# Kernel optimization log

Measured on AMD Instinct MI355X. Metric: run time of the kernel, lower is better.

Reference implementation:

```python
import jax, jax.numpy as jnp
import numpy as np

GROUP_SIZE = 64
SHARED_EXPERT_WEIGHT = 1.0
# FP4 E2M1 codebook: sign bit + {0,.5,1,1.5,2,3,4,6}
FP4_TABLE = jnp.array([0.0, 0.5, 1.0, 1.5, 2.0, 3.0, 4.0, 6.0,
                       -0.0, -0.5, -1.0, -1.5, -2.0, -3.0, -4.0, -6.0], dtype=jnp.float32)


def dequant_fp4(packed, scales, group_size=GROUP_SIZE):
    """packed: [..., K//8, N] int32 (8 nibbles along K per word),
    scales: [..., K//group_size, N] -> dequantized [..., K, N] fp32."""
    shifts = (jnp.arange(8, dtype=jnp.int32) * 4)[:, None]          # [8,1]
    nib = jnp.right_shift(packed[..., :, None, :], shifts) & 0xF     # [..., K//8, 8, N]
    w = FP4_TABLE[nib]
    K = packed.shape[-2] * 8
    w = w.reshape(packed.shape[:-2] + (K, packed.shape[-1]))         # [..., K, N]
    s = jnp.repeat(scales, group_size, axis=-2)                      # [..., K, N]
    return w * s


def setup_inputs() -> dict:
    key = jax.random.key(0)
    ks = jax.random.split(key, 12)
    T, K, I, E, TOPK = 2048, 2048, 1024, 8, 2
    GS = GROUP_SIZE
    MAXI = 2**31 - 1
    u = lambda k, shp: jax.random.uniform(k, shp, jnp.float32, 0.005, 0.02)
    probs = jax.random.uniform(ks[10], (T, TOPK), jnp.float32)
    probs = probs / probs.sum(-1, keepdims=True)
    return {
        "hidden_states": jax.random.normal(ks[0], (T, K), jnp.float32),
        "gate_up_weight_packed": jax.random.randint(ks[1], (E, K // 8, 2 * I), 0, MAXI, jnp.int32),
        "gate_up_scales": u(ks[2], (E, K // GS, 2 * I)),
        "down_weight_packed": jax.random.randint(ks[3], (E, I // 8, K), 0, MAXI, jnp.int32),
        "down_scales": u(ks[4], (E, I // GS, K)),
        "shared_gate_up_packed": jax.random.randint(ks[5], (K // 8, 2 * I), 0, MAXI, jnp.int32),
        "shared_gate_up_scales": u(ks[6], (K // GS, 2 * I)),
        "shared_down_packed": jax.random.randint(ks[7], (I // 8, K), 0, MAXI, jnp.int32),
        "shared_down_scales": u(ks[8], (I // GS, K)),
        "expert_ids": jax.random.randint(ks[9], (T, TOPK), 0, E, jnp.int32),
        "expert_probs": probs,
    }


def reference(hidden_states, gate_up_weight_packed, gate_up_scales,
              down_weight_packed, down_scales,
              shared_gate_up_packed, shared_gate_up_scales,
              shared_down_packed, shared_down_scales,
              expert_ids, expert_probs):
    x = hidden_states                                                # [T, K]
    E = gate_up_weight_packed.shape[0]
    # --- routed experts: dequant + grouped GEMM over all tokens per expert ---
    Wgu = dequant_fp4(gate_up_weight_packed, gate_up_scales)         # [E, K, 2I]
    Wd = dequant_fp4(down_weight_packed, down_scales)                # [E, I, K]
    h = jnp.einsum('tk,ekn->etn', x, Wgu)                            # [E, T, 2I]
    gate, up = jnp.split(h, 2, axis=-1)
    act = jax.nn.silu(gate) * up                                     # [E, T, I]
    y = jnp.einsum('eti,eik->etk', act, Wd)                          # [E, T, K]
    # combine[t,e] = sum over top-k slots routed to e of prob
    one_hot = jax.nn.one_hot(expert_ids, E, dtype=x.dtype)           # [T, topk, E]
    combine = jnp.einsum('tk,tke->te', expert_probs, one_hot)        # [T, E]
    out = jnp.einsum('te,etk->tk', combine, y)                       # [T, K]
    # --- shared expert (always applied, weighted) ---
    Wgu_s = dequant_fp4(shared_gate_up_packed, shared_gate_up_scales)  # [K, 2I]
    Wd_s = dequant_fp4(shared_down_packed, shared_down_scales)         # [I, K]
    hs = x @ Wgu_s
    gs, us = jnp.split(hs, 2, axis=-1)
    shared_out = (jax.nn.silu(gs) * us) @ Wd_s
    return out + SHARED_EXPERT_WEIGHT * shared_out
```

## Files before the change

### kernel.cpp

```cpp
#include <hip/hip_runtime.h>
#include <hip/hip_fp16.h>

#define T_TOK 2048
#define K_DIM 2048
#define I_DIM 1024
#define NE    8
#define TOPK  2
#define GS    64

#define NSLOT  (T_TOK * TOPK)
#define TOTROW (NSLOT + T_TOK)
#define MAXITEM 32

typedef __attribute__((ext_vector_type(8))) _Float16 half8;
typedef __attribute__((ext_vector_type(4))) float f32x4;

#define WS_XB   ((size_t)65536)
#define WS_ACT  (WS_XB  + (size_t)2048 * 2048 * 2)
#define WS_Y    (WS_ACT + (size_t)TOTROW * 1024 * 2)


__device__ __forceinline__ float h2f(ushort h) {
    __half v = *reinterpret_cast<__half*>(&h);
    return __half2float(v);
}

__device__ __forceinline__ void dq_word(unsigned w, __half2 S, unsigned o[4]) {
    unsigned lo  = w & 0x0F0F0F0Fu;
    unsigned hi  = (w >> 4) & 0x0F0F0F0Fu;
    unsigned mlo = lo & 0x07070707u, mhi = hi & 0x07070707u;
    unsigned Hlo = __builtin_amdgcn_perm(0x46444240u, 0x3E3C3800u, mlo)
                 | ((lo & 0x08080808u) << 4);
    unsigned Hhi = __builtin_amdgcn_perm(0x46444240u, 0x3E3C3800u, mhi)
                 | ((hi & 0x08080808u) << 4);
    unsigned e01 = __builtin_amdgcn_perm(Hlo, 0u, 0x05000400u);
    unsigned e23 = __builtin_amdgcn_perm(Hlo, 0u, 0x07000600u);
    unsigned o01 = __builtin_amdgcn_perm(Hhi, 0u, 0x05000400u);
    unsigned o23 = __builtin_amdgcn_perm(Hhi, 0u, 0x07000600u);
    __half2 v0 = __hmul2(*reinterpret_cast<__half2*>(&e01), S);
    __half2 v1 = __hmul2(*reinterpret_cast<__half2*>(&e23), S);
    __half2 v2 = __hmul2(*reinterpret_cast<__half2*>(&o01), S);
    __half2 v3 = __hmul2(*reinterpret_cast<__half2*>(&o23), S);
    o[0] = *reinterpret_cast<unsigned*>(&v0);
    o[1] = *reinterpret_cast<unsigned*>(&v1);
    o[2] = *reinterpret_cast<unsigned*>(&v2);
    o[3] = *reinterpret_cast<unsigned*>(&v3);
}

__device__ __forceinline__ void gld16(const void* g, void* l) {
    __builtin_amdgcn_global_load_lds(
        (const __attribute__((address_space(1))) unsigned*)g,
        (__attribute__((address_space(3))) unsigned*)l, 16, 0, 0);
}

#define PREP_BLK 2048
#define FRONT_GRID (PREP_BLK + 1)

__global__ __launch_bounds__(256) void k_front(
        const float* __restrict__ x, ushort* __restrict__ xb,
        const int* __restrict__ eids,
        int* __restrict__ gcnt, int* __restrict__ gbase,
        int* __restrict__ tileCnt, int* __restrict__ tileE, int* __restrict__ tileM,
        int* __restrict__ tok, int* __restrict__ inv) {
    int id = blockIdx.x;
    int tid = threadIdx.x;

    if (id < PREP_BLK) {
        int idx = id * 256 + tid;
        const float4* p = (const float4*)(x + (size_t)idx * 8);
        float4 f0 = p[0], f1 = p[1];
        __half2 h0 = __floats2half2_rn(f0.x, f0.z);
        __half2 h1 = __floats2half2_rn(f1.x, f1.z);
        __half2 h2 = __floats2half2_rn(f0.y, f0.w);
        __half2 h3 = __floats2half2_rn(f1.y, f1.w);
        unsigned u0 = *reinterpret_cast<unsigned*>(&h0);
        unsigned u1 = *reinterpret_cast<unsigned*>(&h1);
        unsigned u2 = *reinterpret_cast<unsigned*>(&h2);
        unsigned u3 = *reinterpret_cast<unsigned*>(&h3);
        *(int4*)(xb + (size_t)idx * 8) = make_int4(u0, u1, u2, u3);
    } else {
        __shared__ int lcnt[NE], lbase[NE], lcur[NE];
        if (tid < NE) lcnt[tid] = 0;
        __syncthreads();
        for (int i = tid; i < NSLOT; i += 256)
            atomicAdd(&lcnt[eids[i]], 1);
        __syncthreads();
        if (tid == 0) {
            int acc = 0;
            for (int e = 0; e < NE; e++) { lbase[e] = acc; acc += lcnt[e]; }
        }
        __syncthreads();
        if (tid < NE) lcur[tid] = lbase[tid];
        __syncthreads();
        for (int i = tid; i < NSLOT; i += 256) {
            int e = eids[i];
            int pos = atomicAdd(&lcur[e], 1);
            tok[pos] = i >> 1;
            inv[i] = pos;
        }
        for (int t = tid; t < T_TOK; t += 256)
            tok[NSLOT + t] = t;
        if (tid < NE) { gcnt[tid] = lcnt[tid]; gbase[tid] = lbase[tid]; }
        if (tid == 0) {
            gcnt[NE] = T_TOK; gbase[NE] = NSLOT;
            int nt = 0;
            for (int e = 0; e < NE + 1; e++) {
                int c = (e < NE) ? lcnt[e] : T_TOK;
                for (int m = 0; m < c; m += 256) { tileE[nt] = e; tileM[nt] = m; nt++; }
            }
            *tileCnt = nt;
            for (int i = nt; i < 64; i++) { tileE[i] = 0; tileM[i] = 0; }
        }
    }
}

__global__ __launch_bounds__(512) void k_gemm_gateup(
        const ushort* __restrict__ xb,
        const int* __restrict__ gup, const float* __restrict__ gus,
        const int* __restrict__ sup, const float* __restrict__ sus,
        const int* __restrict__ gcnt, const int* __restrict__ gbase,
        const int* __restrict__ tileCnt, const int* __restrict__ tileE,
        const int* __restrict__ tileM,
        const int* __restrict__ tokid, ushort* __restrict__ act) {
    int item = blockIdx.y;
    if (item >= *tileCnt) return;
    int tid = threadIdx.x;
    int e = tileE[item], m0 = tileM[item];
    int cnt = gcnt[e], base = gbase[e];
    int n0 = blockIdx.x * 64;
    const int* wp; const float* sc;
    if (e < NE) { wp = gup + (size_t)e * 256 * 2048; sc = gus + (size_t)e * 32 * 2048; }
    else        { wp = sup; sc = sus; }

    __shared__ __align__(16) ushort xs[256 * 64];
    __shared__ __align__(16) ushort bs[128 * 64];

    int lane = tid & 63, wv = tid >> 6;
    int lid = lane & 15, quad = lane >> 4;
    int wr = wv >> 1, wc = wv & 1;
    int l8 = lane >> 3, l7 = lane & 7;
    int chunk = (l7 ^ l8) * 8;

    const ushort* aSrc[4];
    #pragma unroll
    for (int it = 0; it < 4; it++) {
        int rA = wv * 32 + it * 8 + l8;
        int t = (m0 + rA < cnt) ? tokid[base + m0 + rA] : 0;
        aSrc[it] = xb + (size_t)t * K_DIM + chunk;
    }

    int nloc = tid & 127;
    int kw0 = (tid >> 7) * 2;
    int bj = nloc & 63, bh = nloc >> 6;
    int ncol = (bj < 32) ? (n0 + bh * 32 + bj) : (I_DIM + n0 + bh * 32 + (bj - 32));
    int bd0 = nloc * 64 + ((kw0    ) ^ (nloc & 7)) * 8;
    int bd1 = nloc * 64 + ((kw0 + 1) ^ (nloc & 7)) * 8;

    const int NT = K_DIM / 64;
    const int* wq = wp + (size_t)kw0 * 2048 + ncol;
    const float* sq = sc + ncol;
    unsigned w0 = (unsigned)wq[0];
    unsigned w1 = (unsigned)wq[2048];
    float s = *sq;
    wq += 16384; sq += 2048;

    f32x4 acc[4][4] = {};

    for (int t = 0; t < NT; ++t) {
        #pragma unroll
        for (int it = 0; it < 4; it++) {
            gld16(aSrc[it], &xs[(wv * 4 + it) * 512]);
            aSrc[it] += 64;
        }
        {
            __half2 S = __half2half2(__float2half(s));
            unsigned o[4];
            dq_word(w0, S, o); *(int4*)&bs[bd0] = make_int4(o[0], o[1], o[2], o[3]);
            dq_word(w1, S, o); *(int4*)&bs[bd1] = make_int4(o[0], o[1], o[2], o[3]);
        }
        if (t + 1 < NT) {
            w0 = (unsigned)wq[0];
            w1 = (unsigned)wq[2048];
            s = *sq;
            wq += 16384; sq += 2048;
        }
        __syncthreads();
        __builtin_amdgcn_s_setprio(1);
        #pragma unroll
        for (int ks = 0; ks < 2; ks++) {
            int slot = ((ks * 4 + quad) ^ l7) * 8;
            half8 a[4], b[4];
            #pragma unroll
            for (int mt = 0; mt < 4; mt++)
                a[mt] = *(const half8*)&xs[(wr * 64 + mt * 16 + lid) * 64 + slot];
            #pragma unroll
            for (int nt = 0; nt < 4; nt++)
                b[nt] = *(const half8*)&bs[(wc * 64 + nt * 16 + lid) * 64 + slot];
            #pragma unroll
            for (int mt = 0; mt < 4; mt++)
                #pragma unroll
                for (int nt = 0; nt < 4; nt++)
                    acc[mt][nt] = __builtin_amdgcn_mfma_f32_16x16x32_f16(
                        a[mt], b[nt], acc[mt][nt], 0, 0, 0);
        }
        __builtin_amdgcn_s_setprio(0);
        __syncthreads();
    }

    int c7 = lid & 7;
    int delta = ((c7 >> 1) + ((c7 & 1) << 2)) - c7;
    #pragma unroll
    for (int mt = 0; mt < 4; mt++) {
        #pragma unroll
        for (int i = 0; i < 4; i++) {
            int row = wr * 64 + mt * 16 + quad * 4 + i;
            if (m0 + row < cnt) {
                size_t p = (size_t)(base + m0 + row);
                #pragma unroll
                for (int nt = 0; nt < 2; nt++) {
                    float g = acc[mt][nt][i], u = acc[mt][nt + 2][i];
                    float vv = g / (1.f + __expf(-g)) * u;
                    int ncol2 = n0 + wc * 32 + nt * 16 + lid;
                    __half hb = __float2half(vv);
                    act[p * I_DIM + ncol2 + delta] = *reinterpret_cast<ushort*>(&hb);
                }
            }
        }
    }
}

__global__ __launch_bounds__(512) void k_gemm_down(
        const ushort* __restrict__ actb,
        const int* __restrict__ dwp, const float* __restrict__ dsc,
        const int* __restrict__ sdp, const float* __restrict__ sds,
        const int* __restrict__ gcnt, const int* __restrict__ gbase,
        const int* __restrict__ tileCnt, const int* __restrict__ tileE,
        const int* __restrict__ tileM,
        ushort* __restrict__ y) {
    int item = blockIdx.y;
    if (item >= *tileCnt) return;
    int tid = threadIdx.x;
    int e = tileE[item], m0 = tileM[item];
    int cnt = gcnt[e], base = gbase[e];
    int n0 = blockIdx.x * 128;
    const int* wp; const float* sc;
    if (e < NE) { wp = dwp + (size_t)e * 128 * 2048; sc = dsc + (size_t)e * 16 * 2048; }
    else        { wp = sdp; sc = sds; }

    __shared__ __align__(16) ushort xs[256 * 64];
    __shared__ __align__(16) ushort bs[128 * 64];

    int lane = tid & 63, wv = tid >> 6;
    int lid = lane & 15, quad = lane >> 4;
    int wr = wv >> 1, wc = wv & 1;
    int l8 = lane >> 3, l7 = lane & 7;
    int chunk = (l7 ^ l8) * 8;

    const ushort* aSrc[4];
    #pragma unroll
    for (int it = 0; it < 4; it++) {
        int rA = wv * 32 + it * 8 + l8;
        int rr = m0 + rA; if (rr >= cnt) rr = cnt - 1;
        aSrc[it] = actb + (size_t)(base + rr) * I_DIM + chunk;
    }

    int nloc = tid & 127;
    int kw0 = (tid >> 7) * 2;
    int ncol = n0 + nloc;
    int bd0 = nloc * 64 + ((kw0    ) ^ (nloc & 7)) * 8;
    int bd1 = nloc * 64 + ((kw0 + 1) ^ (nloc & 7)) * 8;

    const int NT = I_DIM / 64;
    const int* wq = wp + (size_t)kw0 * 2048 + ncol;
    const float* sq = sc + ncol;
    unsigned w0 = (unsigned)wq[0];
    unsigned w1 = (unsigned)wq[2048];
    float s = *sq;
    wq += 16384; sq += 2048;

    f32x4 acc[4][4] = {};

    for (int t = 0; t < NT; ++t) {
        #pragma unroll
        for (int it = 0; it < 4; it++) {
            gld16(aSrc[it], &xs[(wv * 4 + it) * 512]);
            aSrc[it] += 64;
        }
        {
            __half2 S = __half2half2(__float2half(s));
            unsigned o[4];
            dq_word(w0, S, o); *(int4*)&bs[bd0] = make_int4(o[0], o[1], o[2], o[3]);
            dq_word(w1, S, o); *(int4*)&bs[bd1] = make_int4(o[0], o[1], o[2], o[3]);
        }
        if (t + 1 < NT) {
            w0 = (unsigned)wq[0];
            w1 = (unsigned)wq[2048];
            s = *sq;
            wq += 16384; sq += 2048;
        }
        __syncthreads();
        __builtin_amdgcn_s_setprio(1);
        #pragma unroll
        for (int ks = 0; ks < 2; ks++) {
            int slot = ((ks * 4 + quad) ^ l7) * 8;
            half8 a[4], b[4];
            #pragma unroll
            for (int mt = 0; mt < 4; mt++)
                a[mt] = *(const half8*)&xs[(wr * 64 + mt * 16 + lid) * 64 + slot];
            #pragma unroll
            for (int nt = 0; nt < 4; nt++)
                b[nt] = *(const half8*)&bs[(wc * 64 + nt * 16 + lid) * 64 + slot];
            #pragma unroll
            for (int mt = 0; mt < 4; mt++)
                #pragma unroll
                for (int nt = 0; nt < 4; nt++)
                    acc[mt][nt] = __builtin_amdgcn_mfma_f32_16x16x32_f16(
                        a[mt], b[nt], acc[mt][nt], 0, 0, 0);
        }
        __builtin_amdgcn_s_setprio(0);
        __syncthreads();
    }

    #pragma unroll
    for (int mt = 0; mt < 4; mt++) {
        #pragma unroll
        for (int i = 0; i < 4; i++) {
            int row = wr * 64 + mt * 16 + quad * 4 + i;
            if (m0 + row < cnt) {
                ushort* yrow = y + (size_t)(base + m0 + row) * 2048 + n0 + wc * 64 + lid;
                #pragma unroll
                for (int nt = 0; nt < 4; nt++) {
                    __half hb = __float2half(acc[mt][nt][i]);
                    yrow[nt * 16] = *reinterpret_cast<ushort*>(&hb);
                }
            }
        }
    }
}

__global__ __launch_bounds__(256) void k_combine(
        const ushort* __restrict__ y, const int* __restrict__ inv,
        const float* __restrict__ prb, float* __restrict__ out) {
    int idx = blockIdx.x * 256 + threadIdx.x;
    int t = idx >> 8;
    int c = (idx & 255) * 8;
    int p0 = inv[2 * t], p1 = inv[2 * t + 1];
    float w0 = prb[2 * t], w1 = prb[2 * t + 1];
    int4 a = *(const int4*)(y + (size_t)p0 * 2048 + c);
    int4 b = *(const int4*)(y + (size_t)p1 * 2048 + c);
    int4 s = *(const int4*)(y + (size_t)(NSLOT + t) * 2048 + c);
    const ushort* au = (const ushort*)&a;
    const ushort* bu = (const ushort*)&b;
    const ushort* su = (const ushort*)&s;
    float o[8];
    #pragma unroll
    for (int j = 0; j < 8; j++)
        o[j] = w0 * h2f(au[j]) + w1 * h2f(bu[j]) + h2f(su[j]);
    *(float4*)(out + (size_t)t * 2048 + c)     = *(float4*)&o[0];
    *(float4*)(out + (size_t)t * 2048 + c + 4) = *(float4*)&o[4];
}

extern "C" void kernel_launch(void* const* d_in, const int* in_sizes, int n_in,
                              void* d_out, int out_size, void* d_ws, size_t ws_size,
                              hipStream_t stream) {
    const float* x    = (const float*)d_in[0];
    const int*   gup  = (const int*)d_in[1];
    const float* gus  = (const float*)d_in[2];
    const int*   dwp  = (const int*)d_in[3];
    const float* dsc  = (const float*)d_in[4];
    const int*   sup  = (const int*)d_in[5];
    const float* sus  = (const float*)d_in[6];
    const int*   sdp  = (const int*)d_in[7];
    const float* sds  = (const float*)d_in[8];
    const int*   eids = (const int*)d_in[9];
    const float* prb  = (const float*)d_in[10];
    float* out = (float*)d_out;

    char*   ws      = (char*)d_ws;
    int*    gcnt    = (int*)(ws + 0);
    int*    gbase   = (int*)(ws + 64);
    int*    tileCnt = (int*)(ws + 128);
    int*    tileE   = (int*)(ws + 192);
    int*    tileM   = (int*)(ws + 448);
    int*    tok     = (int*)(ws + 1024);
    int*    inv     = (int*)(ws + 25600);
    ushort* xb      = (ushort*)(ws + WS_XB);
    ushort* act     = (ushort*)(ws + WS_ACT);
    ushort* y       = (ushort*)(ws + WS_Y);

    k_front<<<FRONT_GRID, 256, 0, stream>>>(
        x, xb, eids, gcnt, gbase, tileCnt, tileE, tileM, tok, inv);
    k_gemm_gateup<<<dim3(I_DIM / 64, MAXITEM), 512, 0, stream>>>(
        xb, gup, gus, sup, sus, gcnt, gbase, tileCnt, tileE, tileM, tok, act);
    k_gemm_down<<<dim3(K_DIM / 128, MAXITEM), 512, 0, stream>>>(
        act, dwp, dsc, sdp, sds, gcnt, gbase, tileCnt, tileE, tileM, y);
    k_combine<<<(T_TOK * K_DIM / 8) / 256, 256, 0, stream>>>(y, inv, prb, out);
}
```

Baseline: 228.9 us.

## Shrink GEMM tiles to 256x64 with 4 waves and move weight prefetch after barrier

Both grouped GEMM kernels change from 512-thread blocks with 256x128 tiles to 256-thread blocks with 256x64 tiles. Each wave now owns 64 rows across the full N width, and the grid doubles along N. The next weight word prefetch is moved after the first barrier into temporaries, with a sched_barrier, so its load latency overlaps the MFMA loop. Smaller tiles and launch_bounds(256,3) aim for more resident blocks and better occupancy, at the cost of reloading A tiles twice as often and dequantizing the same weights less efficiently per FLOP.

Result: slower. 241.2 us (+5.3%).

```diff
diff --git a/kernel.cpp b/kernel.cpp
--- a/kernel.cpp
+++ b/kernel.cpp
@@ -114,7 +114,7 @@
     }
 }
 
-__global__ __launch_bounds__(512) void k_gemm_gateup(
+__global__ __launch_bounds__(256, 3) void k_gemm_gateup(
         const ushort* __restrict__ xb,
         const int* __restrict__ gup, const float* __restrict__ gus,
         const int* __restrict__ sup, const float* __restrict__ sus,
@@ -127,34 +127,32 @@
     int tid = threadIdx.x;
     int e = tileE[item], m0 = tileM[item];
     int cnt = gcnt[e], base = gbase[e];
-    int n0 = blockIdx.x * 64;
+    int n0 = blockIdx.x * 32;
     const int* wp; const float* sc;
     if (e < NE) { wp = gup + (size_t)e * 256 * 2048; sc = gus + (size_t)e * 32 * 2048; }
     else        { wp = sup; sc = sus; }
 
     __shared__ __align__(16) ushort xs[256 * 64];
-    __shared__ __align__(16) ushort bs[128 * 64];
+    __shared__ __align__(16) ushort bs[64 * 64];
 
     int lane = tid & 63, wv = tid >> 6;
     int lid = lane & 15, quad = lane >> 4;
-    int wr = wv >> 1, wc = wv & 1;
     int l8 = lane >> 3, l7 = lane & 7;
     int chunk = (l7 ^ l8) * 8;
 
-    const ushort* aSrc[4];
+    const ushort* aSrc[8];
     #pragma unroll
-    for (int it = 0; it < 4; it++) {
-        int rA = wv * 32 + it * 8 + l8;
+    for (int it = 0; it < 8; it++) {
+        int rA = wv * 64 + it * 8 + l8;
         int t = (m0 + rA < cnt) ? tokid[base + m0 + rA] : 0;
         aSrc[it] = xb + (size_t)t * K_DIM + chunk;
     }
 
-    int nloc = tid & 127;
-    int kw0 = (tid >> 7) * 2;
-    int bj = nloc & 63, bh = nloc >> 6;
-    int ncol = (bj < 32) ? (n0 + bh * 32 + bj) : (I_DIM + n0 + bh * 32 + (bj - 32));
-    int bd0 = nloc * 64 + ((kw0    ) ^ (nloc & 7)) * 8;
-    int bd1 = nloc * 64 + ((kw0 + 1) ^ (nloc & 7)) * 8;
+    int col = tid & 63;
+    int kw0 = (tid >> 6) * 2;
+    int ncol = (col < 32) ? (n0 + col) : (I_DIM + n0 + (col - 32));
+    int bd0 = col * 64 + ((kw0    ) ^ (col & 7)) * 8;
+    int bd1 = col * 64 + ((kw0 + 1) ^ (col & 7)) * 8;
 
     const int NT = K_DIM / 64;
     const int* wq = wp + (size_t)kw0 * 2048 + ncol;
@@ -168,8 +166,8 @@
 
     for (int t = 0; t < NT; ++t) {
         #pragma unroll
-        for (int it = 0; it < 4; it++) {
-            gld16(aSrc[it], &xs[(wv * 4 + it) * 512]);
+        for (int it = 0; it < 8; it++) {
+            gld16(aSrc[it], &xs[(wv * 8 + it) * 512]);
             aSrc[it] += 64;
         }
         {
@@ -178,13 +176,15 @@
             dq_word(w0, S, o); *(int4*)&bs[bd0] = make_int4(o[0], o[1], o[2], o[3]);
             dq_word(w1, S, o); *(int4*)&bs[bd1] = make_int4(o[0], o[1], o[2], o[3]);
         }
+        __syncthreads();
+        unsigned nw0 = w0, nw1 = w1; float ns = s;
         if (t + 1 < NT) {
-            w0 = (unsigned)wq[0];
-            w1 = (unsigned)wq[2048];
-            s = *sq;
+            nw0 = (unsigned)wq[0];
+            nw1 = (unsigned)wq[2048];
+            ns = *sq;
             wq += 16384; sq += 2048;
         }
-        __syncthreads();
+        __builtin_amdgcn_sched_barrier(0);
         __builtin_amdgcn_s_setprio(1);
         #pragma unroll
         for (int ks = 0; ks < 2; ks++) {
@@ -192,10 +192,10 @@
             half8 a[4], b[4];
             #pragma unroll
             for (int mt = 0; mt < 4; mt++)
-                a[mt] = *(const half8*)&xs[(wr * 64 + mt * 16 + lid) * 64 + slot];
+                a[mt] = *(const half8*)&xs[(wv * 64 + mt * 16 + lid) * 64 + slot];
             #pragma unroll
             for (int nt = 0; nt < 4; nt++)
-                b[nt] = *(const half8*)&bs[(wc * 64 + nt * 16 + lid) * 64 + slot];
+                b[nt] = *(const half8*)&bs[(nt * 16 + lid) * 64 + slot];
             #pragma unroll
             for (int mt = 0; mt < 4; mt++)
                 #pragma unroll
@@ -205,6 +205,7 @@
         }
         __builtin_amdgcn_s_setprio(0);
         __syncthreads();
+        w0 = nw0; w1 = nw1; s = ns;
     }
 
     int c7 = lid & 7;
@@ -213,14 +214,14 @@
     for (int mt = 0; mt < 4; mt++) {
         #pragma unroll
         for (int i = 0; i < 4; i++) {
-            int row = wr * 64 + mt * 16 + quad * 4 + i;
+            int row = wv * 64 + mt * 16 + quad * 4 + i;
             if (m0 + row < cnt) {
                 size_t p = (size_t)(base + m0 + row);
                 #pragma unroll
                 for (int nt = 0; nt < 2; nt++) {
                     float g = acc[mt][nt][i], u = acc[mt][nt + 2][i];
                     float vv = g / (1.f + __expf(-g)) * u;
-                    int ncol2 = n0 + wc * 32 + nt * 16 + lid;
+                    int ncol2 = n0 + nt * 16 + lid;
                     __half hb = __float2half(vv);
                     act[p * I_DIM + ncol2 + delta] = *reinterpret_cast<ushort*>(&hb);
                 }
@@ -229,7 +230,7 @@
     }
 }
 
-__global__ __launch_bounds__(512) void k_gemm_down(
+__global__ __launch_bounds__(256, 3) void k_gemm_down(
         const ushort* __restrict__ actb,
         const int* __restrict__ dwp, const float* __restrict__ dsc,
         const int* __restrict__ sdp, const float* __restrict__ sds,
@@ -242,33 +243,32 @@
     int tid = threadIdx.x;
     int e = tileE[item], m0 = tileM[item];
     int cnt = gcnt[e], base = gbase[e];
-    int n0 = blockIdx.x * 128;
+    int n0 = blockIdx.x * 64;
     const int* wp; const float* sc;
     if (e < NE) { wp = dwp + (size_t)e * 128 * 2048; sc = dsc + (size_t)e * 16 * 2048; }
     else        { wp = sdp; sc = sds; }
 
     __shared__ __align__(16) ushort xs[256 * 64];
-    __shared__ __align__(16) ushort bs[128 * 64];
+    __shared__ __align__(16) ushort bs[64 * 64];
 
     int lane = tid & 63, wv = tid >> 6;
     int lid = lane & 15, quad = lane >> 4;
-    int wr = wv >> 1, wc = wv & 1;
     int l8 = lane >> 3, l7 = lane & 7;
     int chunk = (l7 ^ l8) * 8;
 
-    const ushort* aSrc[4];
+    const ushort* aSrc[8];
     #pragma unroll
-    for (int it = 0; it < 4; it++) {
-        int rA = wv * 32 + it * 8 + l8;
+    for (int it = 0; it < 8; it++) {
+        int rA = wv * 64 + it * 8 + l8;
         int rr = m0 + rA; if (rr >= cnt) rr = cnt - 1;
         aSrc[it] = actb + (size_t)(base + rr) * I_DIM + chunk;
     }
 
-    int nloc = tid & 127;
-    int kw0 = (tid >> 7) * 2;
-    int ncol = n0 + nloc;
-    int bd0 = nloc * 64 + ((kw0    ) ^ (nloc & 7)) * 8;
-    int bd1 = nloc * 64 + ((kw0 + 1) ^ (nloc & 7)) * 8;
+    int col = tid & 63;
+    int kw0 = (tid >> 6) * 2;
+    int ncol = n0 + col;
+    int bd0 = col * 64 + ((kw0    ) ^ (col & 7)) * 8;
+    int bd1 = col * 64 + ((kw0 + 1) ^ (col & 7)) * 8;
 
     const int NT = I_DIM / 64;
     const int* wq = wp + (size_t)kw0 * 2048 + ncol;
@@ -282,8 +282,8 @@
 
     for (int t = 0; t < NT; ++t) {
         #pragma unroll
-        for (int it = 0; it < 4; it++) {
-            gld16(aSrc[it], &xs[(wv * 4 + it) * 512]);
+        for (int it = 0; it < 8; it++) {
+            gld16(aSrc[it], &xs[(wv * 8 + it) * 512]);
             aSrc[it] += 64;
         }
         {
@@ -292,13 +292,15 @@
             dq_word(w0, S, o); *(int4*)&bs[bd0] = make_int4(o[0], o[1], o[2], o[3]);
             dq_word(w1, S, o); *(int4*)&bs[bd1] = make_int4(o[0], o[1], o[2], o[3]);
         }
+        __syncthreads();
+        unsigned nw0 = w0, nw1 = w1; float ns = s;
         if (t + 1 < NT) {
-            w0 = (unsigned)wq[0];
-            w1 = (unsigned)wq[2048];
-            s = *sq;
+            nw0 = (unsigned)wq[0];
+            nw1 = (unsigned)wq[2048];
+            ns = *sq;
             wq += 16384; sq += 2048;
         }
-        __syncthreads();
+        __builtin_amdgcn_sched_barrier(0);
         __builtin_amdgcn_s_setprio(1);
         #pragma unroll
         for (int ks = 0; ks < 2; ks++) {
@@ -306,10 +308,10 @@
             half8 a[4], b[4];
             #pragma unroll
             for (int mt = 0; mt < 4; mt++)
-                a[mt] = *(const half8*)&xs[(wr * 64 + mt * 16 + lid) * 64 + slot];
+                a[mt] = *(const half8*)&xs[(wv * 64 + mt * 16 + lid) * 64 + slot];
             #pragma unroll
             for (int nt = 0; nt < 4; nt++)
-                b[nt] = *(const half8*)&bs[(wc * 64 + nt * 16 + lid) * 64 + slot];
+                b[nt] = *(const half8*)&bs[(nt * 16 + lid) * 64 + slot];
             #pragma unroll
             for (int mt = 0; mt < 4; mt++)
                 #pragma unroll
@@ -319,15 +321,16 @@
         }
         __builtin_amdgcn_s_setprio(0);
         __syncthreads();
+        w0 = nw0; w1 = nw1; s = ns;
     }
 
     #pragma unroll
     for (int mt = 0; mt < 4; mt++) {
         #pragma unroll
         for (int i = 0; i < 4; i++) {
-            int row = wr * 64 + mt * 16 + quad * 4 + i;
+            int row = wv * 64 + mt * 16 + quad * 4 + i;
             if (m0 + row < cnt) {
-                ushort* yrow = y + (size_t)(base + m0 + row) * 2048 + n0 + wc * 64 + lid;
+                ushort* yrow = y + (size_t)(base + m0 + row) * 2048 + n0 + lid;
                 #pragma unroll
                 for (int nt = 0; nt < 4; nt++) {
                     __half hb = __float2half(acc[mt][nt][i]);
@@ -390,9 +393,9 @@
 
     k_front<<<FRONT_GRID, 256, 0, stream>>>(
         x, xb, eids, gcnt, gbase, tileCnt, tileE, tileM, tok, inv);
-    k_gemm_gateup<<<dim3(I_DIM / 64, MAXITEM), 512, 0, stream>>>(
+    k_gemm_gateup<<<dim3(I_DIM / 32, MAXITEM), 256, 0, stream>>>(
         xb, gup, gus, sup, sus, gcnt, gbase, tileCnt, tileE, tileM, tok, act);
-    k_gemm_down<<<dim3(K_DIM / 128, MAXITEM), 512, 0, stream>>>(
+    k_gemm_down<<<dim3(K_DIM / 64, MAXITEM), 256, 0, stream>>>(
         act, dwp, dsc, sdp, sds, gcnt, gbase, tileCnt, tileE, tileM, y);
     k_combine<<<(T_TOK * K_DIM / 8) / 256, 256, 0, stream>>>(y, inv, prb, out);
 }
```

## Fuse combine into down GEMM epilogue via weighted atomic adds to output

Applied to the files above, without the earlier changes.

Removes the separate combine kernel and the fp16 intermediate y buffer. The front kernel now zeroes the output and stores a per-row routing weight (1.0 for shared-expert rows). The down GEMM epilogue scatters weighted fp32 atomicAdds directly into the output rows by token id. This saves one kernel launch and the write plus reread of roughly 25 MB of intermediates. In exchange it adds three-way atomic contention per output element, uncoalesced scalar atomics, and a summation order that is no longer deterministic.

Measured after the change: 255.5 us. 1.12x slower.

```diff
diff --git a/kernel.cpp b/kernel.cpp
--- a/kernel.cpp
+++ b/kernel.cpp
@@ -17,13 +17,7 @@
 
 #define WS_XB   ((size_t)65536)
 #define WS_ACT  (WS_XB  + (size_t)2048 * 2048 * 2)
-#define WS_Y    (WS_ACT + (size_t)TOTROW * 1024 * 2)
-
-
-__device__ __forceinline__ float h2f(ushort h) {
-    __half v = *reinterpret_cast<__half*>(&h);
-    return __half2float(v);
-}
+
 
 __device__ __forceinline__ void dq_word(unsigned w, __half2 S, unsigned o[4]) {
     unsigned lo  = w & 0x0F0F0F0Fu;
@@ -58,10 +52,11 @@
 
 __global__ __launch_bounds__(256) void k_front(
         const float* __restrict__ x, ushort* __restrict__ xb,
-        const int* __restrict__ eids,
+        const int* __restrict__ eids, const float* __restrict__ prb,
+        float* __restrict__ out,
         int* __restrict__ gcnt, int* __restrict__ gbase,
         int* __restrict__ tileCnt, int* __restrict__ tileE, int* __restrict__ tileM,
-        int* __restrict__ tok, int* __restrict__ inv) {
+        int* __restrict__ tok, float* __restrict__ wgt) {
     int id = blockIdx.x;
     int tid = threadIdx.x;
 
@@ -78,6 +73,9 @@
         unsigned u2 = *reinterpret_cast<unsigned*>(&h2);
         unsigned u3 = *reinterpret_cast<unsigned*>(&h3);
         *(int4*)(xb + (size_t)idx * 8) = make_int4(u0, u1, u2, u3);
+        float4 z = make_float4(0.f, 0.f, 0.f, 0.f);
+        *(float4*)(out + (size_t)idx * 8)     = z;
+        *(float4*)(out + (size_t)idx * 8 + 4) = z;
     } else {
         __shared__ int lcnt[NE], lbase[NE], lcur[NE];
         if (tid < NE) lcnt[tid] = 0;
@@ -96,10 +94,12 @@
             int e = eids[i];
             int pos = atomicAdd(&lcur[e], 1);
             tok[pos] = i >> 1;
-            inv[i] = pos;
-        }
-        for (int t = tid; t < T_TOK; t += 256)
+            wgt[pos] = prb[i];
+        }
+        for (int t = tid; t < T_TOK; t += 256) {
             tok[NSLOT + t] = t;
+            wgt[NSLOT + t] = 1.0f;
+        }
         if (tid < NE) { gcnt[tid] = lcnt[tid]; gbase[tid] = lbase[tid]; }
         if (tid == 0) {
             gcnt[NE] = T_TOK; gbase[NE] = NSLOT;
@@ -236,7 +236,8 @@
         const int* __restrict__ gcnt, const int* __restrict__ gbase,
         const int* __restrict__ tileCnt, const int* __restrict__ tileE,
         const int* __restrict__ tileM,
-        ushort* __restrict__ y) {
+        const int* __restrict__ tokid, const float* __restrict__ wgt,
+        float* __restrict__ out) {
     int item = blockIdx.y;
     if (item >= *tileCnt) return;
     int tid = threadIdx.x;
@@ -327,37 +328,16 @@
         for (int i = 0; i < 4; i++) {
             int row = wr * 64 + mt * 16 + quad * 4 + i;
             if (m0 + row < cnt) {
-                ushort* yrow = y + (size_t)(base + m0 + row) * 2048 + n0 + wc * 64 + lid;
+                int p = base + m0 + row;
+                int tkn = tokid[p];
+                float w = wgt[p];
+                float* orow = out + (size_t)tkn * 2048 + n0 + wc * 64 + lid;
                 #pragma unroll
-                for (int nt = 0; nt < 4; nt++) {
-                    __half hb = __float2half(acc[mt][nt][i]);
-                    yrow[nt * 16] = *reinterpret_cast<ushort*>(&hb);
-                }
+                for (int nt = 0; nt < 4; nt++)
+                    atomicAdd(&orow[nt * 16], w * acc[mt][nt][i]);
             }
         }
     }
-}
-
-__global__ __launch_bounds__(256) void k_combine(
-        const ushort* __restrict__ y, const int* __restrict__ inv,
-        const float* __restrict__ prb, float* __restrict__ out) {
-    int idx = blockIdx.x * 256 + threadIdx.x;
-    int t = idx >> 8;
-    int c = (idx & 255) * 8;
-    int p0 = inv[2 * t], p1 = inv[2 * t + 1];
-    float w0 = prb[2 * t], w1 = prb[2 * t + 1];
-    int4 a = *(const int4*)(y + (size_t)p0 * 2048 + c);
-    int4 b = *(const int4*)(y + (size_t)p1 * 2048 + c);
-    int4 s = *(const int4*)(y + (size_t)(NSLOT + t) * 2048 + c);
-    const ushort* au = (const ushort*)&a;
-    const ushort* bu = (const ushort*)&b;
-    const ushort* su = (const ushort*)&s;
-    float o[8];
-    #pragma unroll
-    for (int j = 0; j < 8; j++)
-        o[j] = w0 * h2f(au[j]) + w1 * h2f(bu[j]) + h2f(su[j]);
-    *(float4*)(out + (size_t)t * 2048 + c)     = *(float4*)&o[0];
-    *(float4*)(out + (size_t)t * 2048 + c + 4) = *(float4*)&o[4];
 }
 
 extern "C" void kernel_launch(void* const* d_in, const int* in_sizes, int n_in,
@@ -383,16 +363,14 @@
     int*    tileE   = (int*)(ws + 192);
     int*    tileM   = (int*)(ws + 448);
     int*    tok     = (int*)(ws + 1024);
-    int*    inv     = (int*)(ws + 25600);
+    float*  wgt     = (float*)(ws + 25600);
     ushort* xb      = (ushort*)(ws + WS_XB);
     ushort* act     = (ushort*)(ws + WS_ACT);
-    ushort* y       = (ushort*)(ws + WS_Y);
 
     k_front<<<FRONT_GRID, 256, 0, stream>>>(
-        x, xb, eids, gcnt, gbase, tileCnt, tileE, tileM, tok, inv);
+        x, xb, eids, prb, out, gcnt, gbase, tileCnt, tileE, tileM, tok, wgt);
     k_gemm_gateup<<<dim3(I_DIM / 64, MAXITEM), 512, 0, stream>>>(
         xb, gup, gus, sup, sus, gcnt, gbase, tileCnt, tileE, tileM, tok, act);
     k_gemm_down<<<dim3(K_DIM / 128, MAXITEM), 512, 0, stream>>>(
-        act, dwp, dsc, sdp, sds, gcnt, gbase, tileCnt, tileE, tileM, y);
-    k_combine<<<(T_TOK * K_DIM / 8) / 256, 256, 0, stream>>>(y, inv, prb, out);
-}
+        act, dwp, dsc, sdp, sds, gcnt, gbase, tileCnt, tileE, tileM, tok, wgt, out);
+}
```

## Fuse all MoE stages into one cooperative persistent kernel with grid syncs

Applied to the files above, without the earlier changes.

Replaces the four separate launches (convert/route, gate-up GEMM, down GEMM, combine) with a single cooperative kernel of 512 blocks that separates the stages with grid.sync. Each block handles one tile item per GEMM phase (bid>>4 indexes the item), and the conversion and combine phases use grid-stride loops. The aim is to remove launch gaps and tail effects between kernels. In exchange, the grid is capped at 512 blocks, which limits parallelism per phase, and it adds the cost of grid-wide barriers. If the cooperative launch fails, it falls back to the old four-kernel path.

New measurement: 429.2 us. 87.5% more time.

```diff
diff --git a/kernel.cpp b/kernel.cpp
--- a/kernel.cpp
+++ b/kernel.cpp
@@ -1,5 +1,8 @@
 #include <hip/hip_runtime.h>
 #include <hip/hip_fp16.h>
+#include <hip/hip_cooperative_groups.h>
+
+namespace cg = cooperative_groups;
 
 #define T_TOK 2048
 #define K_DIM 2048
@@ -53,6 +56,303 @@
         (__attribute__((address_space(3))) unsigned*)l, 16, 0, 0);
 }
 
+#define FGRID 512
+
+__global__ __launch_bounds__(512, 4) void k_fused(
+        const float* __restrict__ x,
+        const int* __restrict__ gup, const float* __restrict__ gus,
+        const int* __restrict__ dwp, const float* __restrict__ dsc,
+        const int* __restrict__ sup, const float* __restrict__ sus,
+        const int* __restrict__ sdp, const float* __restrict__ sds,
+        const int* __restrict__ eids, const float* __restrict__ prb,
+        float* __restrict__ out,
+        ushort* __restrict__ xb, ushort* __restrict__ act, ushort* __restrict__ y,
+        int* __restrict__ gcnt, int* __restrict__ gbase,
+        int* __restrict__ tileCnt, int* __restrict__ tileE, int* __restrict__ tileM,
+        int* __restrict__ tok, int* __restrict__ inv) {
+    cg::grid_group grid = cg::this_grid();
+    const int bid = blockIdx.x;
+    const int tid = threadIdx.x;
+
+    __shared__ __align__(16) ushort xs[256 * 64];
+    __shared__ __align__(16) ushort bs[128 * 64];
+
+    for (int idx = bid * 512 + tid; idx < T_TOK * K_DIM / 8; idx += FGRID * 512) {
+        const float4* p = (const float4*)(x + (size_t)idx * 8);
+        float4 f0 = p[0], f1 = p[1];
+        __half2 h0 = __floats2half2_rn(f0.x, f0.z);
+        __half2 h1 = __floats2half2_rn(f1.x, f1.z);
+        __half2 h2 = __floats2half2_rn(f0.y, f0.w);
+        __half2 h3 = __floats2half2_rn(f1.y, f1.w);
+        *(int4*)(xb + (size_t)idx * 8) = make_int4(
+            *reinterpret_cast<unsigned*>(&h0), *reinterpret_cast<unsigned*>(&h1),
+            *reinterpret_cast<unsigned*>(&h2), *reinterpret_cast<unsigned*>(&h3));
+    }
+    if (bid == 0) {
+        int* lcnt  = (int*)xs;
+        int* lbase = lcnt + 8;
+        int* lcur  = lbase + 8;
+        if (tid < NE) lcnt[tid] = 0;
+        __syncthreads();
+        for (int i = tid; i < NSLOT; i += 512)
+            atomicAdd(&lcnt[eids[i]], 1);
+        __syncthreads();
+        if (tid == 0) {
+            int acc = 0;
+            for (int e = 0; e < NE; e++) { lbase[e] = acc; acc += lcnt[e]; }
+        }
+        __syncthreads();
+        if (tid < NE) lcur[tid] = lbase[tid];
+        __syncthreads();
+        for (int i = tid; i < NSLOT; i += 512) {
+            int e = eids[i];
+            int pos = atomicAdd(&lcur[e], 1);
+            tok[pos] = i >> 1;
+            inv[i] = pos;
+        }
+        for (int t = tid; t < T_TOK; t += 512)
+            tok[NSLOT + t] = t;
+        if (tid < NE) { gcnt[tid] = lcnt[tid]; gbase[tid] = lbase[tid]; }
+        if (tid == 0) {
+            gcnt[NE] = T_TOK; gbase[NE] = NSLOT;
+            int nt = 0;
+            for (int e = 0; e < NE + 1; e++) {
+                int c = (e < NE) ? lcnt[e] : T_TOK;
+                for (int m = 0; m < c; m += 256) { tileE[nt] = e; tileM[nt] = m; nt++; }
+            }
+            *tileCnt = nt;
+            for (int i = nt; i < 64; i++) { tileE[i] = 0; tileM[i] = 0; }
+        }
+    }
+    grid.sync();
+
+    {
+        int item = bid >> 4;
+        if (item < *tileCnt) {
+            int e = tileE[item], m0 = tileM[item];
+            int cnt = gcnt[e], base = gbase[e];
+            int n0 = (bid & 15) * 64;
+            const int* wp; const float* sc;
+            if (e < NE) { wp = gup + (size_t)e * 256 * 2048; sc = gus + (size_t)e * 32 * 2048; }
+            else        { wp = sup; sc = sus; }
+
+            int lane = tid & 63, wv = tid >> 6;
+            int lid = lane & 15, quad = lane >> 4;
+            int wr = wv >> 1, wc = wv & 1;
+            int l8 = lane >> 3, l7 = lane & 7;
+            int chunk = (l7 ^ l8) * 8;
+
+            const ushort* aSrc[4];
+            #pragma unroll
+            for (int it = 0; it < 4; it++) {
+                int rA = wv * 32 + it * 8 + l8;
+                int t = (m0 + rA < cnt) ? tok[base + m0 + rA] : 0;
+                aSrc[it] = xb + (size_t)t * K_DIM + chunk;
+            }
+
+            int nloc = tid & 127;
+            int kw0 = (tid >> 7) * 2;
+            int bj = nloc & 63, bh = nloc >> 6;
+            int ncol = (bj < 32) ? (n0 + bh * 32 + bj) : (I_DIM + n0 + bh * 32 + (bj - 32));
+            int bd0 = nloc * 64 + ((kw0    ) ^ (nloc & 7)) * 8;
+            int bd1 = nloc * 64 + ((kw0 + 1) ^ (nloc & 7)) * 8;
+
+            const int NT = K_DIM / 64;
+            const int* wq = wp + (size_t)kw0 * 2048 + ncol;
+            const float* sq = sc + ncol;
+            unsigned w0 = (unsigned)wq[0];
+            unsigned w1 = (unsigned)wq[2048];
+            float s = *sq;
+            wq += 16384; sq += 2048;
+
+            f32x4 acc[4][4] = {};
+
+            for (int t = 0; t < NT; ++t) {
+                #pragma unroll
+                for (int it = 0; it < 4; it++) {
+                    gld16(aSrc[it], &xs[(wv * 4 + it) * 512]);
+                    aSrc[it] += 64;
+                }
+                {
+                    __half2 S = __half2half2(__float2half(s));
+                    unsigned o[4];
+                    dq_word(w0, S, o); *(int4*)&bs[bd0] = make_int4(o[0], o[1], o[2], o[3]);
+                    dq_word(w1, S, o); *(int4*)&bs[bd1] = make_int4(o[0], o[1], o[2], o[3]);
+                }
+                if (t + 1 < NT) {
+                    w0 = (unsigned)wq[0];
+                    w1 = (unsigned)wq[2048];
+                    s = *sq;
+                    wq += 16384; sq += 2048;
+                }
+                __syncthreads();
+                __builtin_amdgcn_s_setprio(1);
+                #pragma unroll
+                for (int ks = 0; ks < 2; ks++) {
+                    int slot = ((ks * 4 + quad) ^ l7) * 8;
+                    half8 a[4], b[4];
+                    #pragma unroll
+                    for (int mt = 0; mt < 4; mt++)
+                        a[mt] = *(const half8*)&xs[(wr * 64 + mt * 16 + lid) * 64 + slot];
+                    #pragma unroll
+                    for (int nt = 0; nt < 4; nt++)
+                        b[nt] = *(const half8*)&bs[(wc * 64 + nt * 16 + lid) * 64 + slot];
+                    #pragma unroll
+                    for (int mt = 0; mt < 4; mt++)
+                        #pragma unroll
+                        for (int nt = 0; nt < 4; nt++)
+                            acc[mt][nt] = __builtin_amdgcn_mfma_f32_16x16x32_f16(
+                                a[mt], b[nt], acc[mt][nt], 0, 0, 0);
+                }
+                __builtin_amdgcn_s_setprio(0);
+                __syncthreads();
+            }
+
+            int c7 = lid & 7;
+            int delta = ((c7 >> 1) + ((c7 & 1) << 2)) - c7;
+            #pragma unroll
+            for (int mt = 0; mt < 4; mt++) {
+                #pragma unroll
+                for (int i = 0; i < 4; i++) {
+                    int row = wr * 64 + mt * 16 + quad * 4 + i;
+                    if (m0 + row < cnt) {
+                        size_t p = (size_t)(base + m0 + row);
+                        #pragma unroll
+                        for (int nt = 0; nt < 2; nt++) {
+                            float g = acc[mt][nt][i], u = acc[mt][nt + 2][i];
+                            float vv = g / (1.f + __expf(-g)) * u;
+                            int ncol2 = n0 + wc * 32 + nt * 16 + lid;
+                            __half hb = __float2half(vv);
+                            act[p * I_DIM + ncol2 + delta] = *reinterpret_cast<ushort*>(&hb);
+                        }
+                    }
+                }
+            }
+        }
+    }
+    grid.sync();
+
+    {
+        int item = bid >> 4;
+        if (item < *tileCnt) {
+            int e = tileE[item], m0 = tileM[item];
+            int cnt = gcnt[e], base = gbase[e];
+            int n0 = (bid & 15) * 128;
+            const int* wp; const float* sc;
+            if (e < NE) { wp = dwp + (size_t)e * 128 * 2048; sc = dsc + (size_t)e * 16 * 2048; }
+            else        { wp = sdp; sc = sds; }
+
+            int lane = tid & 63, wv = tid >> 6;
+            int lid = lane & 15, quad = lane >> 4;
+            int wr = wv >> 1, wc = wv & 1;
+            int l8 = lane >> 3, l7 = lane & 7;
+            int chunk = (l7 ^ l8) * 8;
+
+            const ushort* aSrc[4];
+            #pragma unroll
+            for (int it = 0; it < 4; it++) {
+                int rA = wv * 32 + it * 8 + l8;
+                int rr = m0 + rA; if (rr >= cnt) rr = cnt - 1;
+                aSrc[it] = act + (size_t)(base + rr) * I_DIM + chunk;
+            }
+
+            int nloc = tid & 127;
+            int kw0 = (tid >> 7) * 2;
+            int ncol = n0 + nloc;
+            int bd0 = nloc * 64 + ((kw0    ) ^ (nloc & 7)) * 8;
+            int bd1 = nloc * 64 + ((kw0 + 1) ^ (nloc & 7)) * 8;
+
+            const int NT = I_DIM / 64;
+            const int* wq = wp + (size_t)kw0 * 2048 + ncol;
+            const float* sq = sc + ncol;
+            unsigned w0 = (unsigned)wq[0];
+            unsigned w1 = (unsigned)wq[2048];
+            float s = *sq;
+            wq += 16384; sq += 2048;
+
+            f32x4 acc[4][4] = {};
+
+            for (int t = 0; t < NT; ++t) {
+                #pragma unroll
+                for (int it = 0; it < 4; it++) {
+                    gld16(aSrc[it], &xs[(wv * 4 + it) * 512]);
+                    aSrc[it] += 64;
+                }
+                {
+                    __half2 S = __half2half2(__float2half(s));
+                    unsigned o[4];
+                    dq_word(w0, S, o); *(int4*)&bs[bd0] = make_int4(o[0], o[1], o[2], o[3]);
+                    dq_word(w1, S, o); *(int4*)&bs[bd1] = make_int4(o[0], o[1], o[2], o[3]);
+                }
+                if (t + 1 < NT) {
+                    w0 = (unsigned)wq[0];
+                    w1 = (unsigned)wq[2048];
+                    s = *sq;
+                    wq += 16384; sq += 2048;
+                }
+                __syncthreads();
+                __builtin_amdgcn_s_setprio(1);
+                #pragma unroll
+                for (int ks = 0; ks < 2; ks++) {
+                    int slot = ((ks * 4 + quad) ^ l7) * 8;
+                    half8 a[4], b[4];
+                    #pragma unroll
+                    for (int mt = 0; mt < 4; mt++)
+                        a[mt] = *(const half8*)&xs[(wr * 64 + mt * 16 + lid) * 64 + slot];
+                    #pragma unroll
+                    for (int nt = 0; nt < 4; nt++)
+                        b[nt] = *(const half8*)&bs[(wc * 64 + nt * 16 + lid) * 64 + slot];
+                    #pragma unroll
+                    for (int mt = 0; mt < 4; mt++)
+                        #pragma unroll
+                        for (int nt = 0; nt < 4; nt++)
+                            acc[mt][nt] = __builtin_amdgcn_mfma_f32_16x16x32_f16(
+                                a[mt], b[nt], acc[mt][nt], 0, 0, 0);
+                }
+                __builtin_amdgcn_s_setprio(0);
+                __syncthreads();
+            }
+
+            #pragma unroll
+            for (int mt = 0; mt < 4; mt++) {
+                #pragma unroll
+                for (int i = 0; i < 4; i++) {
+                    int row = wr * 64 + mt * 16 + quad * 4 + i;
+                    if (m0 + row < cnt) {
+                        ushort* yrow = y + (size_t)(base + m0 + row) * 2048 + n0 + wc * 64 + lid;
+                        #pragma unroll
+                        for (int nt = 0; nt < 4; nt++) {
+                            __half hb = __float2half(acc[mt][nt][i]);
+                            yrow[nt * 16] = *reinterpret_cast<ushort*>(&hb);
+                        }
+                    }
+                }
+            }
+        }
+    }
+    grid.sync();
+
+    for (int idx = bid * 512 + tid; idx < T_TOK * K_DIM / 8; idx += FGRID * 512) {
+        int t = idx >> 8;
+        int c = (idx & 255) * 8;
+        int p0 = inv[2 * t], p1 = inv[2 * t + 1];
+        float w0 = prb[2 * t], w1 = prb[2 * t + 1];
+        int4 a = *(const int4*)(y + (size_t)p0 * 2048 + c);
+        int4 b = *(const int4*)(y + (size_t)p1 * 2048 + c);
+        int4 sv = *(const int4*)(y + (size_t)(NSLOT + t) * 2048 + c);
+        const ushort* au = (const ushort*)&a;
+        const ushort* bu = (const ushort*)&b;
+        const ushort* su = (const ushort*)&sv;
+        float o[8];
+        #pragma unroll
+        for (int j = 0; j < 8; j++)
+            o[j] = w0 * h2f(au[j]) + w1 * h2f(bu[j]) + h2f(su[j]);
+        *(float4*)(out + (size_t)t * 2048 + c)     = *(float4*)&o[0];
+        *(float4*)(out + (size_t)t * 2048 + c + 4) = *(float4*)&o[4];
+    }
+}
+
+
 #define PREP_BLK 2048
 #define FRONT_GRID (PREP_BLK + 1)
 
@@ -73,11 +373,9 @@
         __half2 h1 = __floats2half2_rn(f1.x, f1.z);
         __half2 h2 = __floats2half2_rn(f0.y, f0.w);
         __half2 h3 = __floats2half2_rn(f1.y, f1.w);
-        unsigned u0 = *reinterpret_cast<unsigned*>(&h0);
-        unsigned u1 = *reinterpret_cast<unsigned*>(&h1);
-        unsigned u2 = *reinterpret_cast<unsigned*>(&h2);
-        unsigned u3 = *reinterpret_cast<unsigned*>(&h3);
-        *(int4*)(xb + (size_t)idx * 8) = make_int4(u0, u1, u2, u3);
+        *(int4*)(xb + (size_t)idx * 8) = make_int4(
+            *reinterpret_cast<unsigned*>(&h0), *reinterpret_cast<unsigned*>(&h1),
+            *reinterpret_cast<unsigned*>(&h2), *reinterpret_cast<unsigned*>(&h3));
     } else {
         __shared__ int lcnt[NE], lbase[NE], lcur[NE];
         if (tid < NE) lcnt[tid] = 0;
@@ -388,11 +686,24 @@
     ushort* act     = (ushort*)(ws + WS_ACT);
     ushort* y       = (ushort*)(ws + WS_Y);
 
-    k_front<<<FRONT_GRID, 256, 0, stream>>>(
-        x, xb, eids, gcnt, gbase, tileCnt, tileE, tileM, tok, inv);
-    k_gemm_gateup<<<dim3(I_DIM / 64, MAXITEM), 512, 0, stream>>>(
-        xb, gup, gus, sup, sus, gcnt, gbase, tileCnt, tileE, tileM, tok, act);
-    k_gemm_down<<<dim3(K_DIM / 128, MAXITEM), 512, 0, stream>>>(
-        act, dwp, dsc, sdp, sds, gcnt, gbase, tileCnt, tileE, tileM, y);
-    k_combine<<<(T_TOK * K_DIM / 8) / 256, 256, 0, stream>>>(y, inv, prb, out);
-}
+    void* args[] = {
+        (void*)&x, (void*)&gup, (void*)&gus, (void*)&dwp, (void*)&dsc,
+        (void*)&sup, (void*)&sus, (void*)&sdp, (void*)&sds,
+        (void*)&eids, (void*)&prb, (void*)&out,
+        (void*)&xb, (void*)&act, (void*)&y,
+        (void*)&gcnt, (void*)&gbase, (void*)&tileCnt, (void*)&tileE, (void*)&tileM,
+        (void*)&tok, (void*)&inv
+    };
+    hipError_t rc = hipLaunchCooperativeKernel(
+        (const void*)k_fused, dim3(FGRID), dim3(512), args, 0, stream);
+    if (rc != hipSuccess) {
+        (void)hipGetLastError();
+        k_front<<<FRONT_GRID, 256, 0, stream>>>(
+            x, xb, eids, gcnt, gbase, tileCnt, tileE, tileM, tok, inv);
+        k_gemm_gateup<<<dim3(I_DIM / 64, MAXITEM), 512, 0, stream>>>(
+            xb, gup, gus, sup, sus, gcnt, gbase, tileCnt, tileE, tileM, tok, act);
+        k_gemm_down<<<dim3(K_DIM / 128, MAXITEM), 512, 0, stream>>>(
+            act, dwp, dsc, sdp, sds, gcnt, gbase, tileCnt, tileE, tileM, y);
+        k_combine<<<(T_TOK * K_DIM / 8) / 256, 256, 0, stream>>>(y, inv, prb, out);
+    }
+}
```
